# Kernel optimization log

Measured on AMD Instinct MI355X. Metric: run time of the kernel, lower is better.

The kernel has to match this reference:

```python
import jax, jax.numpy as jnp
import numpy as np
import math

B, S, K, D, H, LH, W, L = 8, 2048, 128, 512, 8, 4, 128, 4
DH = D // H           # 64, head dim
NW = S // W           # 16 windows
NUM_STEPS = 1000
RESCALE = 4000.0


def setup_inputs() -> dict:
    key = jax.random.key(0)
    ks = iter(jax.random.split(key, 48))
    def rn(shape, s=0.02):
        return jax.random.normal(next(ks), shape, dtype=jnp.float32) * s
    return {
        "x": jax.random.normal(next(ks), (B, S, K), dtype=jnp.float32),
        "t": jax.random.randint(next(ks), (B,), 0, NUM_STEPS, dtype=jnp.int32),
        "token_w": rn((K, D)), "token_b": jnp.zeros((D,), jnp.float32),
        "ax1": rn((NW, D), 1.0), "ax2": rn((W, D), 1.0),
        "time_w1": rn((D, 4 * D)), "time_b1": jnp.zeros((4 * D,), jnp.float32),
        "time_w2": rn((4 * D, D)), "time_b2": jnp.zeros((D,), jnp.float32),
        "ln1_g": jnp.ones((L, D), jnp.float32), "ln1_b": jnp.zeros((L, D), jnp.float32),
        "wq": rn((L, D, D)), "wk": rn((L, D, D)), "wv": rn((L, D, D)),
        "wo": rn((L, D, D)), "wo_b": jnp.zeros((L, D), jnp.float32),
        "ln2_g": jnp.ones((L, D), jnp.float32), "ln2_b": jnp.zeros((L, D), jnp.float32),
        "ff_w1": rn((L, D, 4 * D)), "ff_b1": jnp.zeros((L, 4 * D), jnp.float32),
        "ff_w2": rn((L, 4 * D, D)), "ff_b2": jnp.zeros((L, D), jnp.float32),
        "norm_g": jnp.ones((D,), jnp.float32), "norm_b": jnp.zeros((D,), jnp.float32),
        "out_w": rn((D, K)), "out_b": jnp.zeros((K,), jnp.float32),
        "alpha": jax.random.normal(next(ks), (1,), dtype=jnp.float32),
    }


def _layernorm(x, g, b, eps=1e-5):
    mu = x.mean(-1, keepdims=True)
    var = ((x - mu) ** 2).mean(-1, keepdims=True)
    return (x - mu) * jax.lax.rsqrt(var + eps) * g + b


def _mish(x):
    return x * jnp.tanh(jax.nn.softplus(x))


def _sinusoidal(t):
    # SinusoidalPosEmb(dim=D, num_steps=NUM_STEPS, rescale_steps=4000)
    tt = t.astype(jnp.float32) / NUM_STEPS * RESCALE
    half = D // 2
    freqs = jnp.exp(jnp.arange(half, dtype=jnp.float32) * (-math.log(10000.0) / (half - 1)))
    e = tt[:, None] * freqs[None, :]
    return jnp.concatenate([jnp.sin(e), jnp.cos(e)], axis=-1)  # (B, D)


def _linear_attn(q, k, v):
    # non-causal kernelized linear attention; q,k,v: (B, h, S, dh)
    scale = DH ** -0.25
    q = jax.nn.softmax(q * scale, axis=-1)   # softmax over feature dim
    k = jax.nn.softmax(k * scale, axis=-2)   # softmax over sequence dim
    ctx = jnp.einsum('bhnd,bhne->bhde', k, v)
    return jnp.einsum('bhnd,bhde->bhne', q, ctx)


def _local_attn(q, k, v):
    # windowed softmax attention, window W, look_backward=1, look_forward=1
    b, h = q.shape[0], q.shape[1]
    qw = q.reshape(b, h, NW, W, DH) * (DH ** -0.5)
    def look_around(x):
        xw = x.reshape(b, h, NW, W, DH)
        xp = jnp.pad(xw, ((0, 0), (0, 0), (1, 1), (0, 0), (0, 0)))
        # keys of windows [i-1, i, i+1] -> (b, h, NW, 3W, dh)
        return jnp.concatenate([xp[:, :, :-2], xp[:, :, 1:-1], xp[:, :, 2:]], axis=3)
    kw, vw = look_around(k), look_around(v)
    win = jnp.arange(NW)[:, None] + (jnp.arange(3 * W) // W)[None, :] - 1  # (NW, 3W)
    valid = (win >= 0) & (win < NW)
    dots = jnp.einsum('bhnwd,bhnkd->bhnwk', qw, kw)
    mask_value = -jnp.finfo(dots.dtype).max
    dots = jnp.where(valid[None, None, :, None, :], dots, mask_value)
    attn = jax.nn.softmax(dots, axis=-1)
    out = jnp.einsum('bhnwk,bhnkd->bhnwd', attn, vw)
    return out.reshape(b, h, S, DH)


def reference(x, t, token_w, token_b, ax1, ax2, time_w1, time_b1, time_w2, time_b2,
              ln1_g, ln1_b, wq, wk, wv, wo, wo_b, ln2_g, ln2_b,
              ff_w1, ff_b1, ff_w2, ff_b2, norm_g, norm_b, out_w, out_b, alpha):
    te = _sinusoidal(t)
    te = _mish(te @ time_w1 + time_b1) @ time_w2 + time_b2          # (B, D)
    h = x @ token_w + token_b                                        # token embedding
    pos = (ax1[:, None, :] + ax2[None, :, :]).reshape(S, D)          # axial pos emb (summed)
    h = h + pos[None] + te[:, None, :]
    for l in range(L):
        n = _layernorm(h, ln1_g[l], ln1_b[l])
        def split_heads(y):
            return y.reshape(B, S, H, DH).transpose(0, 2, 1, 3)
        q = split_heads(n @ wq[l]); k = split_heads(n @ wk[l]); v = split_heads(n @ wv[l])
        lo = _local_attn(q[:, :LH], k[:, :LH], v[:, :LH])            # local heads first
        gl = _linear_attn(q[:, LH:], k[:, LH:], v[:, LH:])           # global linear-attn heads
        a = jnp.concatenate([lo, gl], axis=1).transpose(0, 2, 1, 3).reshape(B, S, D)
        h = h + a @ wo[l] + wo_b[l]
        n = _layernorm(h, ln2_g[l], ln2_b[l])
        h = h + jax.nn.gelu(n @ ff_w1[l] + ff_b1[l], approximate=False) @ ff_w2[l] + ff_b2[l]
    out = _layernorm(h, norm_g, norm_b) @ out_w + out_b              # (B, S, K)
    return alpha * out.transpose(0, 2, 1)                            # permute + Rezero -> (B, K, S)
```

## Files before the change

### kernel.cpp

```cpp
#include <hip/hip_runtime.h>

typedef __bf16 bf16;
typedef float f32x4 __attribute__((ext_vector_type(4)));
typedef __bf16 b8v __attribute__((ext_vector_type(8)));
typedef __bf16 b4v __attribute__((ext_vector_type(4)));

#define S_LEN 2048
#define DMODEL 512
#define KDIM 128
#define NWIN 16
#define WIN 128
#define QKVS 1536

__device__ inline f32x4 mfma16(b8v a, b8v b, f32x4 c) {
  return __builtin_amdgcn_mfma_f32_16x16x32_bf16(a, b, c, 0, 0, 0);
}

__device__ inline void gload16(const bf16* g, bf16* l) {
  __builtin_amdgcn_global_load_lds(
      (const __attribute__((address_space(1))) void*)g,
      (__attribute__((address_space(3))) void*)l, 16, 0, 0);
}


__global__ __launch_bounds__(256) void conv_kernel(const float* __restrict__ in, bf16* __restrict__ out, int n) {
  int i4 = (blockIdx.x * 256 + threadIdx.x) * 4;
  if (i4 < n) {
    float4 v = *(const float4*)(in + i4);
    b4v o; o[0] = (bf16)v.x; o[1] = (bf16)v.y; o[2] = (bf16)v.z; o[3] = (bf16)v.w;
    *(b4v*)(out + i4) = o;
  }
}

__global__ __launch_bounds__(256) void convT_kernel(const float* __restrict__ W, bf16* __restrict__ WT,
                                                    int Kd, int N, size_t in_ls, size_t out_ls) {
  __shared__ float tile[32][33];
  int k0 = blockIdx.x * 32, n0 = blockIdx.y * 32;
  const float* Wl = W + (size_t)blockIdx.z * in_ls;
  bf16* WTl = WT + (size_t)blockIdx.z * out_ls;
  int tx = threadIdx.x & 31, ty = threadIdx.x >> 5;
  #pragma unroll
  for (int i = 0; i < 4; i++)
    tile[ty + i*8][tx] = Wl[(size_t)(k0 + ty + i*8) * N + n0 + tx];
  __syncthreads();
  #pragma unroll
  for (int i = 0; i < 4; i++)
    WTl[(size_t)(n0 + ty + i*8) * Kd + k0 + tx] = (bf16)tile[tx][ty + i*8];
}


__global__ __launch_bounds__(256) void time1_kernel(const int* __restrict__ t,
    const float* __restrict__ w1, const float* __restrict__ b1, float* __restrict__ te1) {
  __shared__ float te[512];
  __shared__ float red[4][64];
  int b = blockIdx.x >> 5;
  int c0 = (blockIdx.x & 31) * 64;
  int tid = threadIdx.x;
  float tt = (float)t[b] * 4.0f;
  {
    float fr = expf((float)tid * (-9.210340371976184f / 255.0f));
    float e = tt * fr;
    te[tid] = sinf(e);
    te[tid + 256] = cosf(e);
  }
  __syncthreads();
  int lane = tid & 63, wv = tid >> 6;
  float acc = 0.f;
  const float* wcol = w1 + (size_t)(wv * 128) * 2048 + c0 + lane;
  for (int dd = 0; dd < 128; dd++) acc = fmaf(te[wv * 128 + dd], wcol[(size_t)dd * 2048], acc);
  red[wv][lane] = acc;
  __syncthreads();
  if (tid < 64) {
    float a = red[0][tid] + red[1][tid] + red[2][tid] + red[3][tid] + b1[c0 + tid];
    float sp = (a > 20.f) ? a : log1pf(expf(a));
    te1[b * 2048 + c0 + tid] = a * tanhf(sp);
  }
}

__global__ __launch_bounds__(256) void time2_kernel(const float* __restrict__ te1,
    const float* __restrict__ w2, const float* __restrict__ b2, float* __restrict__ te2) {
  __shared__ float hb[2048];
  __shared__ float red[4][64];
  int b = blockIdx.x >> 3;
  int c0 = (blockIdx.x & 7) * 64;
  int tid = threadIdx.x;
  for (int i = tid; i < 2048; i += 256) hb[i] = te1[b * 2048 + i];
  __syncthreads();
  int lane = tid & 63, wv = tid >> 6;
  float acc = 0.f;
  const float* wcol = w2 + (size_t)(wv * 512) * 512 + c0 + lane;
  for (int dd = 0; dd < 512; dd++) acc = fmaf(hb[wv * 512 + dd], wcol[(size_t)dd * 512], acc);
  red[wv][lane] = acc;
  __syncthreads();
  if (tid < 64)
    te2[b * 512 + c0 + tid] = red[0][tid] + red[1][tid] + red[2][tid] + red[3][tid] + b2[c0 + tid];
}


__global__ __launch_bounds__(256) void ln_kernel(const float* __restrict__ hsrc,
    const float* __restrict__ gg, const float* __restrict__ bb, bf16* __restrict__ out) {
  int row = blockIdx.x * 4 + (threadIdx.x >> 6);
  int lane = threadIdx.x & 63;
  const float* hr = hsrc + (size_t)row * 512 + lane * 8;
  float4 v0 = *(const float4*)hr;
  float4 v1 = *(const float4*)(hr + 4);
  float xv[8] = {v0.x, v0.y, v0.z, v0.w, v1.x, v1.y, v1.z, v1.w};
  float s = 0.f;
  #pragma unroll
  for (int j = 0; j < 8; j++) s += xv[j];
  #pragma unroll
  for (int off = 1; off < 64; off <<= 1) s += __shfl_xor(s, off);
  float mu = s * (1.f / 512.f);
  float vs = 0.f;
  #pragma unroll
  for (int j = 0; j < 8; j++) { float dd = xv[j] - mu; vs += dd * dd; }
  #pragma unroll
  for (int off = 1; off < 64; off <<= 1) vs += __shfl_xor(vs, off);
  float rstd = 1.f / sqrtf(vs * (1.f / 512.f) + 1e-5f);
  int dbase = lane * 8;
  bf16* orow = out + (size_t)row * 512 + dbase;
  #pragma unroll
  for (int j = 0; j < 8; j++)
    orow[j] = (bf16)((xv[j] - mu) * rstd * gg[dbase + j] + bb[dbase + j]);
}

template<int EPI>
__global__ __launch_bounds__(256) void gemm_kernel(
    const bf16* __restrict__ A, const bf16* __restrict__ BT,
    const float* __restrict__ bias, float* __restrict__ Cf, bf16* __restrict__ Cb,
    int N, int Kd, int nbx,
    const float* __restrict__ q1, const float* __restrict__ q2, const float* __restrict__ q3,
    const float* __restrict__ alphap) {
  __shared__ bf16 As[2][4096];
  __shared__ bf16 Bs[2][4096];
  int tid = threadIdx.x;
  int lane = tid & 63, wid = tid >> 6;
  int g = lane >> 4, lr = lane & 15;
  int wm = wid >> 1, wn = wid & 1;
  int p = blockIdx.x;
  int cpx = (int)gridDim.x >> 3;
  int vid = (p & 7) * cpx + (p >> 3);
  int m0 = (vid / nbx) * 128;
  int n0 = (vid % nbx) * 128;
  f32x4 acc[4][4] = {};
  int srow = wid * 16 + (lane >> 2);
  int scol = (lane & 3) * 8;
  const bf16* pa = A + (size_t)(m0 + srow) * Kd + scol;
  const bf16* pb = BT + (size_t)(n0 + srow) * Kd + scol;
  const size_t rstep = (size_t)64 * Kd;
  int nt = Kd >> 5;
  auto stage = [&](int buf, int k0) {
    bf16* lA = &As[buf][wid * 512];
    bf16* lB = &Bs[buf][wid * 512];
    gload16(pa + k0, lA);
    gload16(pa + rstep + k0, lA + 2048);
    gload16(pb + k0, lB);
    gload16(pb + rstep + k0, lB + 2048);
  };
  stage(0, 0);
  __syncthreads();
  int cur = 0;
  for (int t = 0; t < nt; ++t) {
    if (t + 1 < nt) stage(cur ^ 1, (t + 1) * 32);
    b8v af[4], bfv[4];
    #pragma unroll
    for (int i = 0; i < 4; i++) af[i]  = *(const b8v*)&As[cur][(wm * 64 + i * 16 + lr) * 32 + g * 8];
    #pragma unroll
    for (int i = 0; i < 4; i++) bfv[i] = *(const b8v*)&Bs[cur][(wn * 64 + i * 16 + lr) * 32 + g * 8];
    #pragma unroll
    for (int mf = 0; mf < 4; mf++)
      #pragma unroll
      for (int nf = 0; nf < 4; nf++)
        acc[mf][nf] = mfma16(af[mf], bfv[nf], acc[mf][nf]);
    __syncthreads();
    cur ^= 1;
  }
  if constexpr (EPI == 4) {
    __shared__ float Ts[32][130];
    float alp = alphap[0];
    int b_ = m0 >> 11, sb = m0 & 2047;
    #pragma unroll
    for (int cg = 0; cg < 4; cg++) {
      __syncthreads();
      if (wn == (cg >> 1)) {
        #pragma unroll
        for (int nfi = 0; nfi < 2; nfi++) {
          int nf = (cg & 1) * 2 + nfi;
          int cl = nfi * 16 + lr;
          float bv = bias[cg * 32 + cl];
          #pragma unroll
          for (int mf = 0; mf < 4; mf++)
            #pragma unroll
            for (int r = 0; r < 4; r++)
              Ts[cl][wm * 64 + mf * 16 + g * 4 + r] = alp * (acc[mf][nf][r] + bv);
        }
      }
      __syncthreads();
      int cl = tid >> 3, soff = (tid & 7) * 16;
      int col = cg * 32 + cl;
      float* dst = Cf + (size_t)b_ * (KDIM * S_LEN) + (size_t)col * S_LEN + sb + soff;
      #pragma unroll
      for (int q4 = 0; q4 < 4; q4++) {
        float4 v = {Ts[cl][soff + q4*4], Ts[cl][soff + q4*4 + 1], Ts[cl][soff + q4*4 + 2], Ts[cl][soff + q4*4 + 3]};
        *(float4*)(dst + q4 * 4) = v;
      }
    }
    return;
  }
  #pragma unroll
  for (int mf = 0; mf < 4; mf++) {
    #pragma unroll
    for (int nf = 0; nf < 4; nf++) {
      int col = n0 + wn * 64 + nf * 16 + lr;
      float bv = (EPI != 0) ? bias[col] : 0.0f;
      #pragma unroll
      for (int r = 0; r < 4; r++) {
        int row = m0 + wm * 64 + mf * 16 + g * 4 + r;
        float v = acc[mf][nf][r] + bv;
        if (EPI == 0) {
          Cb[(size_t)row * N + col] = (bf16)v;
        } else if (EPI == 2) {
          Cf[(size_t)row * N + col] += v;
        } else if (EPI == 3) {
          float ge = 0.5f * v * (1.0f + erff(v * 0.70710678118654752f));
          Cb[(size_t)row * N + col] = (bf16)ge;
        } else if (EPI == 5) {
          int b_ = row >> 11, s_ = row & 2047;
          float pv = q1[(s_ >> 7) * 512 + col] + q2[(s_ & 127) * 512 + col] + q3[b_ * 512 + col];
          Cf[(size_t)row * N + col] = v + pv;
        }
      }
    }
  }
}

__global__ __launch_bounds__(256) void locattn_kernel(
    const bf16* __restrict__ qkv, bf16* __restrict__ ab) {
  __shared__ bf16 Ks[128][72];
  __shared__ bf16 Vt[64][136];
  __shared__ bf16 Ps[4][32][136];
  int w = blockIdx.x;
  int b = blockIdx.y >> 2, hh = blockIdx.y & 3;
  int tid = threadIdx.x, wid = tid >> 6, lane = tid & 63;
  int g = lane >> 4, lr = lane & 15;
  const size_t rowb = (size_t)b * S_LEN * QKVS;
  int qrow0 = w * WIN + wid * 32;
  b8v qf[2][2];
  #pragma unroll
  for (int mf = 0; mf < 2; mf++)
    #pragma unroll
    for (int kf = 0; kf < 2; kf++)
      qf[mf][kf] = *(const b8v*)(qkv + rowb + (size_t)(qrow0 + mf * 16 + lr) * QKVS + hh * 64 + kf * 32 + g * 8);
  float mrun[2][4], lrun[2][4];
  f32x4 oacc[2][4] = {};
  #pragma unroll
  for (int mf = 0; mf < 2; mf++)
    #pragma unroll
    for (int r = 0; r < 4; r++) { mrun[mf][r] = -3e38f; lrun[mf][r] = 0.f; }
  for (int c = 0; c < 3; c++) {
    int wc = w - 1 + c;
    if (wc < 0 || wc >= NWIN) continue;
    __syncthreads();
    {
      int row = tid >> 1, f0 = (tid & 1) * 32;
      const bf16* kp = qkv + rowb + (size_t)(wc * WIN + row) * QKVS + 512 + hh * 64 + f0;
      #pragma unroll
      for (int i = 0; i < 4; i++)
        *(b8v*)&Ks[row][f0 + i * 8] = *(const b8v*)(kp + i * 8);
      const bf16* vp = qkv + rowb + (size_t)(wc * WIN + row) * QKVS + 1024 + hh * 64 + f0;
      #pragma unroll
      for (int i = 0; i < 4; i++) {
        b8v vv = *(const b8v*)(vp + i * 8);
        #pragma unroll
        for (int j = 0; j < 8; j++) Vt[f0 + i * 8 + j][row] = vv[j];
      }
    }
    __syncthreads();
    f32x4 sc[2][8] = {};
    #pragma unroll
    for (int nf = 0; nf < 8; nf++) {
      #pragma unroll
      for (int kf = 0; kf < 2; kf++) {
        b8v kfr = *(const b8v*)&Ks[nf * 16 + lr][kf * 32 + g * 8];
        sc[0][nf] = mfma16(qf[0][kf], kfr, sc[0][nf]);
        sc[1][nf] = mfma16(qf[1][kf], kfr, sc[1][nf]);
      }
    }
    #pragma unroll
    for (int mf = 0; mf < 2; mf++) {
      #pragma unroll
      for (int r = 0; r < 4; r++) {
        float cm = -3e38f;
        #pragma unroll
        for (int nf = 0; nf < 8; nf++) { sc[mf][nf][r] *= 0.125f; cm = fmaxf(cm, sc[mf][nf][r]); }
        cm = fmaxf(cm, __shfl_xor(cm, 1));
        cm = fmaxf(cm, __shfl_xor(cm, 2));
        cm = fmaxf(cm, __shfl_xor(cm, 4));
        cm = fmaxf(cm, __shfl_xor(cm, 8));
        float mnew = fmaxf(mrun[mf][r], cm);
        float corr = __expf(mrun[mf][r] - mnew);
        float rs = 0.f;
        #pragma unroll
        for (int nf = 0; nf < 8; nf++) { float p = __expf(sc[mf][nf][r] - mnew); sc[mf][nf][r] = p; rs += p; }
        rs += __shfl_xor(rs, 1); rs += __shfl_xor(rs, 2);
        rs += __shfl_xor(rs, 4); rs += __shfl_xor(rs, 8);
        lrun[mf][r] = lrun[mf][r] * corr + rs;
        mrun[mf][r] = mnew;
        #pragma unroll
        for (int vf = 0; vf < 4; vf++) oacc[mf][vf][r] *= corr;
      }
    }
    #pragma unroll
    for (int mf = 0; mf < 2; mf++)
      #pragma unroll
      for (int nf = 0; nf < 8; nf++)
        #pragma unroll
        for (int r = 0; r < 4; r++)
          Ps[wid][mf * 16 + g * 4 + r][nf * 16 + lr] = (bf16)sc[mf][nf][r];
    #pragma unroll
    for (int kf2 = 0; kf2 < 4; kf2++) {
      b8v pa0 = *(const b8v*)&Ps[wid][lr][kf2 * 32 + g * 8];
      b8v pa1 = *(const b8v*)&Ps[wid][16 + lr][kf2 * 32 + g * 8];
      #pragma unroll
      for (int vf = 0; vf < 4; vf++) {
        b8v vv = *(const b8v*)&Vt[vf * 16 + lr][kf2 * 32 + g * 8];
        oacc[0][vf] = mfma16(pa0, vv, oacc[0][vf]);
        oacc[1][vf] = mfma16(pa1, vv, oacc[1][vf]);
      }
    }
  }
  #pragma unroll
  for (int mf = 0; mf < 2; mf++) {
    #pragma unroll
    for (int r = 0; r < 4; r++) {
      float inv = 1.0f / lrun[mf][r];
      int row = qrow0 + mf * 16 + g * 4 + r;
      #pragma unroll
      for (int vf = 0; vf < 4; vf++)
        ab[(size_t)b * S_LEN * DMODEL + (size_t)row * DMODEL + hh * 64 + vf * 16 + lr] = (bf16)(oacc[mf][vf][r] * inv);
    }
  }
}


__global__ __launch_bounds__(256) void la2_kernel(const bf16* __restrict__ qkv,
    float* __restrict__ part, float* __restrict__ psum) {
  int ch = blockIdx.x, bh = blockIdx.y;
  int b = bh >> 2, hh = bh & 3;
  __shared__ float ke[128][65];
  __shared__ float vsh[128][65];
  __shared__ float red[4][64];
  int tid = threadIdx.x;
  const float scale = 0.35355339059327373f;
  const size_t base = ((size_t)b * S_LEN + (size_t)ch * 128) * QKVS;
  const bf16* kp = qkv + base + 768 + hh * 64;
  const bf16* vp = qkv + base + 1280 + hh * 64;
  for (int i = tid; i < 1024; i += 256) {
    int s = i >> 3, d0 = (i & 7) * 8;
    b8v kv = *(const b8v*)(kp + (size_t)s * QKVS + d0);
    b8v vv = *(const b8v*)(vp + (size_t)s * QKVS + d0);
    #pragma unroll
    for (int j = 0; j < 8; j++) {
      ke[s][d0 + j] = __expf((float)kv[j] * scale);
      vsh[s][d0 + j] = (float)vv[j];
    }
  }
  __syncthreads();
  int d = tid & 63, sg = tid >> 6;
  float ps = 0.f;
  for (int s = sg * 32; s < sg * 32 + 32; s++) ps += ke[s][d];
  red[sg][d] = ps;
  int e = tid & 63, dg = tid >> 6;
  float accv[16] = {};
  for (int s = 0; s < 128; s++) {
    float vv2 = vsh[s][e];
    #pragma unroll
    for (int i = 0; i < 16; i++) accv[i] = fmaf(ke[s][dg * 16 + i], vv2, accv[i]);
  }
  __syncthreads();
  float* pp = part + ((size_t)ch * 32 + bh) * 4096 + (size_t)dg * 16 * 64 + e;
  #pragma unroll
  for (int i = 0; i < 16; i++) pp[i * 64] = accv[i];
  if (tid < 64)
    psum[((size_t)ch * 32 + bh) * 64 + tid] = red[0][tid] + red[1][tid] + red[2][tid] + red[3][tid];
}

__global__ __launch_bounds__(256) void la2b_kernel(const float* __restrict__ part,
    const float* __restrict__ psum, float* __restrict__ ctx) {
  int idx = blockIdx.x * 256 + threadIdx.x;
  int bh = idx >> 12;
  int d = (idx >> 6) & 63;
  float s = 0.f, cs = 0.f;
  for (int c = 0; c < 16; c++) {
    s += part[(size_t)c * 131072 + idx];
    cs += psum[(size_t)(c * 32 + bh) * 64 + d];
  }
  ctx[idx] = s / cs;
}

__global__ __launch_bounds__(256) void la3_kernel(const bf16* __restrict__ qkv,
    const float* __restrict__ ctx, bf16* __restrict__ ab) {
  int ch = blockIdx.x, bh = blockIdx.y;
  int b = bh >> 2, hh = bh & 3;
  __shared__ float cs[64][65];
  int tid = threadIdx.x;
  for (int i = tid; i < 4096; i += 256) cs[i >> 6][i & 63] = ctx[(size_t)bh * 4096 + i];
  __syncthreads();
  int s = ch * 128 + (tid >> 1);
  int e0 = (tid & 1) * 32;
  const float scale = 0.35355339059327373f;
  const bf16* qr = qkv + ((size_t)b * S_LEN + s) * QKVS + 256 + hh * 64;
  float qv[64];
  float mx = -3e38f;
  #pragma unroll
  for (int i = 0; i < 8; i++) {
    b8v qq = *(const b8v*)(qr + i * 8);
    #pragma unroll
    for (int j = 0; j < 8; j++) { qv[i * 8 + j] = (float)qq[j] * scale; mx = fmaxf(mx, qv[i * 8 + j]); }
  }
  float sum = 0.f;
  #pragma unroll
  for (int dd = 0; dd < 64; dd++) { qv[dd] = __expf(qv[dd] - mx); sum += qv[dd]; }
  float inv = 1.f / sum;
  float o[32] = {};
  #pragma unroll
  for (int dd = 0; dd < 64; dd++) {
    float qq = qv[dd] * inv;
    #pragma unroll
    for (int j = 0; j < 32; j++) o[j] = fmaf(qq, cs[dd][e0 + j], o[j]);
  }
  bf16* op = ab + ((size_t)b * S_LEN + s) * DMODEL + 256 + hh * 64 + e0;
  #pragma unroll
  for (int j = 0; j < 32; j++) op[j] = (bf16)o[j];
}


extern "C" void kernel_launch(void* const* d_in, const int* in_sizes, int n_in,
                              void* d_out, int out_size, void* d_ws, size_t ws_size,
                              hipStream_t stream) {
  (void)in_sizes; (void)n_in; (void)out_size; (void)ws_size;
  const float* x_f     = (const float*)d_in[0];
  const int*   t_i     = (const int*)  d_in[1];
  const float* token_w = (const float*)d_in[2];
  const float* token_b = (const float*)d_in[3];
  const float* ax1     = (const float*)d_in[4];
  const float* ax2     = (const float*)d_in[5];
  const float* time_w1 = (const float*)d_in[6];
  const float* time_b1 = (const float*)d_in[7];
  const float* time_w2 = (const float*)d_in[8];
  const float* time_b2 = (const float*)d_in[9];
  const float* ln1_g   = (const float*)d_in[10];
  const float* ln1_b   = (const float*)d_in[11];
  const float* wq      = (const float*)d_in[12];
  const float* wk      = (const float*)d_in[13];
  const float* wv      = (const float*)d_in[14];
  const float* wo      = (const float*)d_in[15];
  const float* wo_b    = (const float*)d_in[16];
  const float* ln2_g   = (const float*)d_in[17];
  const float* ln2_b   = (const float*)d_in[18];
  const float* ff_w1   = (const float*)d_in[19];
  const float* ff_b1   = (const float*)d_in[20];
  const float* ff_w2   = (const float*)d_in[21];
  const float* ff_b2   = (const float*)d_in[22];
  const float* norm_g  = (const float*)d_in[23];
  const float* norm_b  = (const float*)d_in[24];
  const float* out_w   = (const float*)d_in[25];
  const float* out_b   = (const float*)d_in[26];
  const float* alpha   = (const float*)d_in[27];

  char* ws = (char*)d_ws;
  float* h      = (float*)(ws + 0);
  float* te1    = (float*)(ws + 33554432);
  float* te2    = (float*)(ws + 33619968);
  float* psum   = (float*)(ws + 33636352);
  float* ctx    = (float*)(ws + 33767424);
  float* part   = (float*)(ws + 34291712);
  bf16* nbuf    = (bf16*)(ws + 42680320);
  bf16* qkvb    = (bf16*)(ws + 59457536);
  bf16* abuf    = (bf16*)(ws + 109789184);
  bf16* gbuf    = qkvb;
  bf16* xw      = (bf16*)(ws + 126566400);
  bf16* token_wT= (bf16*)(ws + 130760704);
  bf16* wqkvT   = (bf16*)(ws + 130891776);
  bf16* woT     = (bf16*)(ws + 137183232);
  bf16* ff1T    = (bf16*)(ws + 139280384);
  bf16* ff2T    = (bf16*)(ws + 147668992);
  bf16* outwT   = (bf16*)(ws + 156057600);

  conv_kernel<<<2048, 256, 0, stream>>>(x_f, xw, 2097152);
  convT_kernel<<<dim3(4, 16, 1),  256, 0, stream>>>(token_w, token_wT, 128, 512, 65536, 65536);
  convT_kernel<<<dim3(16, 16, 4), 256, 0, stream>>>(wq, wqkvT,           512, 512, 262144, 786432);
  convT_kernel<<<dim3(16, 16, 4), 256, 0, stream>>>(wk, wqkvT + 262144,  512, 512, 262144, 786432);
  convT_kernel<<<dim3(16, 16, 4), 256, 0, stream>>>(wv, wqkvT + 524288,  512, 512, 262144, 786432);
  convT_kernel<<<dim3(16, 16, 4), 256, 0, stream>>>(wo, woT, 512, 512, 262144, 262144);
  convT_kernel<<<dim3(16, 64, 4), 256, 0, stream>>>(ff_w1, ff1T, 512, 2048, 1048576, 1048576);
  convT_kernel<<<dim3(64, 16, 4), 256, 0, stream>>>(ff_w2, ff2T, 2048, 512, 1048576, 1048576);
  convT_kernel<<<dim3(16, 4, 1),  256, 0, stream>>>(out_w, outwT, 512, 128, 65536, 65536);

  time1_kernel<<<256, 256, 0, stream>>>(t_i, time_w1, time_b1, te1);
  time2_kernel<<<64, 256, 0, stream>>>(te1, time_w2, time_b2, te2);

  gemm_kernel<5><<<512, 256, 0, stream>>>(xw, token_wT, token_b, h, nullptr, 512, 128, 4, ax1, ax2, te2, nullptr);

  for (int l = 0; l < 4; l++) {
    ln_kernel<<<4096, 256, 0, stream>>>(h, ln1_g + l * 512, ln1_b + l * 512, nbuf);
    gemm_kernel<0><<<1536, 256, 0, stream>>>(nbuf, wqkvT + (size_t)l * 786432, nullptr, nullptr, qkvb, 1536, 512, 12, nullptr, nullptr, nullptr, nullptr);
    locattn_kernel<<<dim3(16, 32), 256, 0, stream>>>(qkvb, abuf);
    la2_kernel<<<dim3(16, 32), 256, 0, stream>>>(qkvb, part, psum);
    la2b_kernel<<<512, 256, 0, stream>>>(part, psum, ctx);
    la3_kernel<<<dim3(16, 32), 256, 0, stream>>>(qkvb, ctx, abuf);
    gemm_kernel<2><<<512, 256, 0, stream>>>(abuf, woT + (size_t)l * 262144, wo_b + l * 512, h, nullptr, 512, 512, 4, nullptr, nullptr, nullptr, nullptr);
    ln_kernel<<<4096, 256, 0, stream>>>(h, ln2_g + l * 512, ln2_b + l * 512, nbuf);
    gemm_kernel<3><<<2048, 256, 0, stream>>>(nbuf, ff1T + (size_t)l * 1048576, ff_b1 + l * 2048, nullptr, gbuf, 2048, 512, 16, nullptr, nullptr, nullptr, nullptr);
    gemm_kernel<2><<<512, 256, 0, stream>>>(gbuf, ff2T + (size_t)l * 1048576, ff_b2 + l * 512, h, nullptr, 512, 2048, 4, nullptr, nullptr, nullptr, nullptr);
  }

  ln_kernel<<<4096, 256, 0, stream>>>(h, norm_g, norm_b, nbuf);
  gemm_kernel<4><<<128, 256, 0, stream>>>(nbuf, outwT, out_b, (float*)d_out, nullptr, 128, 512, 1, nullptr, nullptr, nullptr, alpha);
}
```

Before: 1.212 ms.

## Add larger-tile 512-thread GEMM with triple-buffered async LDS pipeline

Adds a new templated GEMM that uses 8 waves per block, bigger output tiles (128x256 or 256x256) and a three-stage global-to-LDS ring buffer. It relies on raw vmcnt waits and a single barrier per K step, with XOR-swizzled LDS addressing and raised wave priority around the MFMA block. The per-layer QKV, output projection and FFN GEMMs are moved onto it, while the old GEMM is kept only for the embedding and output epilogues. The aim is to cut barrier and load latency stalls and raise data reuse per tile. In exchange, per-thread register use is higher and the grids are smaller, which can lower occupancy or leave CUs idle at the tail.

New measurement: 1.109 ms. 8.5% less time.

```diff
diff --git a/kernel.cpp b/kernel.cpp
--- a/kernel.cpp
+++ b/kernel.cpp
@@ -21,6 +21,10 @@
       (const __attribute__((address_space(1))) void*)g,
       (__attribute__((address_space(3))) void*)l, 16, 0, 0);
 }
+
+template<int N>
+__device__ inline void waitvm() { asm volatile("s_waitcnt vmcnt(%0)" :: "n"(N) : "memory"); }
+__device__ inline void barrier_raw() { asm volatile("s_barrier" ::: "memory"); }
 
 
 __global__ __launch_bounds__(256) void conv_kernel(const float* __restrict__ in, bf16* __restrict__ out, int n) {
@@ -122,6 +126,100 @@
   #pragma unroll
   for (int j = 0; j < 8; j++)
     orow[j] = (bf16)((xv[j] - mu) * rstd * gg[dbase + j] + bb[dbase + j]);
+}
+
+template<int EPI, int BM, int BN>
+__global__ __launch_bounds__(512, 2) void gemm2_kernel(
+    const bf16* __restrict__ A, const bf16* __restrict__ BT,
+    const float* __restrict__ bias, float* __restrict__ Cf, bf16* __restrict__ Cb,
+    int N, int Kd, int nbx) {
+  constexpr int LA = BM / 128;
+  constexpr int LB = BN / 128;
+  constexpr int LPI = LA + LB;
+  constexpr int EA = BM * 32;
+  constexpr int EB = BN * 32;
+  constexpr int ER = EA + EB;
+  constexpr int MF = BM / 32;
+  constexpr int NF = BN / 64;
+  __shared__ bf16 lds[ER * 3];
+  int tid = threadIdx.x;
+  int lane = tid & 63, wid = tid >> 6;
+  int g = lane >> 4, lr = lane & 15;
+  int wm = wid >> 2, wn = wid & 3;
+  int p = blockIdx.x;
+  int cpx = (int)gridDim.x >> 3;
+  int vid = (p & 7) * cpx + (p >> 3);
+  int m0 = (vid / nbx) * BM;
+  int n0 = (vid % nbx) * BN;
+  f32x4 acc[MF][NF] = {};
+  int rl = tid >> 2;
+  int csw = ((tid & 3) ^ ((rl >> 1) & 3)) * 8;
+  const bf16* pa = A + (size_t)(m0 + rl) * Kd + csw;
+  const bf16* pb = BT + (size_t)(n0 + rl) * Kd + csw;
+  int NT = Kd >> 5;
+  auto stage = [&](int t, int buf) {
+    int k0 = t << 5;
+    bf16* base = lds + buf * ER + (wid << 9);
+    #pragma unroll
+    for (int rr = 0; rr < LA; rr++)
+      gload16(pa + (size_t)(rr * 128) * Kd + k0, base + rr * 4096);
+    #pragma unroll
+    for (int rr = 0; rr < LB; rr++)
+      gload16(pb + (size_t)(rr * 128) * Kd + k0, base + EA + rr * 4096);
+  };
+  stage(0, 0);
+  stage(1, 1);
+  waitvm<LPI>();
+  barrier_raw();
+  for (int t = 0; t < NT; ++t) {
+    if (t + 2 < NT) stage(t + 2, (t + 2) % 3);
+    const bf16* ba = lds + (t % 3) * ER;
+    const bf16* bb = ba + EA;
+    b8v af[MF], bfr[NF];
+    #pragma unroll
+    for (int i = 0; i < MF; i++) {
+      int ra = wm * (BM / 2) + i * 16 + lr;
+      af[i] = *(const b8v*)(ba + ra * 32 + ((g * 8) ^ (((ra >> 1) & 3) << 3)));
+    }
+    #pragma unroll
+    for (int j = 0; j < NF; j++) {
+      int rb = wn * (BN / 4) + j * 16 + lr;
+      bfr[j] = *(const b8v*)(bb + rb * 32 + ((g * 8) ^ (((rb >> 1) & 3) << 3)));
+    }
+    __builtin_amdgcn_s_setprio(1);
+    #pragma unroll
+    for (int i = 0; i < MF; i++)
+      #pragma unroll
+      for (int j = 0; j < NF; j++)
+        acc[i][j] = mfma16(af[i], bfr[j], acc[i][j]);
+    __builtin_amdgcn_s_setprio(0);
+    if (t + 1 < NT) {
+      if (t + 2 < NT) waitvm<LPI>();
+      else            waitvm<0>();
+      barrier_raw();
+    }
+  }
+  #pragma unroll
+  for (int i = 0; i < MF; i++) {
+    #pragma unroll
+    for (int j = 0; j < NF; j++) {
+      int col = n0 + wn * (BN / 4) + j * 16 + lr;
+      float bv = (EPI != 0) ? bias[col] : 0.0f;
+      #pragma unroll
+      for (int r = 0; r < 4; r++) {
+        int row = m0 + wm * (BM / 2) + i * 16 + g * 4 + r;
+        float v = acc[i][j][r] + bv;
+        if (EPI == 0) {
+          Cb[(size_t)row * N + col] = (bf16)v;
+        } else if (EPI == 2) {
+          Cf[(size_t)row * N + col] += v;
+        } else if (EPI == 3) {
+          float ge = 0.5f * v * (1.0f + erff(v * 0.70710678118654752f));
+          Cb[(size_t)row * N + col] = (bf16)ge;
+        }
+      }
+    }
+  }
 }
 
 template<int EPI>
@@ -212,19 +310,12 @@
     #pragma unroll
     for (int nf = 0; nf < 4; nf++) {
       int col = n0 + wn * 64 + nf * 16 + lr;
-      float bv = (EPI != 0) ? bias[col] : 0.0f;
+      float bv = bias[col];
       #pragma unroll
       for (int r = 0; r < 4; r++) {
         int row = m0 + wm * 64 + mf * 16 + g * 4 + r;
         float v = acc[mf][nf][r] + bv;
-        if (EPI == 0) {
-          Cb[(size_t)row * N + col] = (bf16)v;
-        } else if (EPI == 2) {
-          Cf[(size_t)row * N + col] += v;
-        } else if (EPI == 3) {
-          float ge = 0.5f * v * (1.0f + erff(v * 0.70710678118654752f));
-          Cb[(size_t)row * N + col] = (bf16)ge;
-        } else if (EPI == 5) {
+        if (EPI == 5) {
           int b_ = row >> 11, s_ = row & 2047;
           float pv = q1[(s_ >> 7) * 512 + col] + q2[(s_ & 127) * 512 + col] + q3[b_ * 512 + col];
           Cf[(size_t)row * N + col] = v + pv;
@@ -504,15 +595,15 @@
 
   for (int l = 0; l < 4; l++) {
     ln_kernel<<<4096, 256, 0, stream>>>(h, ln1_g + l * 512, ln1_b + l * 512, nbuf);
-    gemm_kernel<0><<<1536, 256, 0, stream>>>(nbuf, wqkvT + (size_t)l * 786432, nullptr, nullptr, qkvb, 1536, 512, 12, nullptr, nullptr, nullptr, nullptr);
+    gemm2_kernel<0, 128, 256><<<768, 512, 0, stream>>>(nbuf, wqkvT + (size_t)l * 786432, nullptr, nullptr, qkvb, 1536, 512, 6);
     locattn_kernel<<<dim3(16, 32), 256, 0, stream>>>(qkvb, abuf);
     la2_kernel<<<dim3(16, 32), 256, 0, stream>>>(qkvb, part, psum);
     la2b_kernel<<<512, 256, 0, stream>>>(part, psum, ctx);
     la3_kernel<<<dim3(16, 32), 256, 0, stream>>>(qkvb, ctx, abuf);
-    gemm_kernel<2><<<512, 256, 0, stream>>>(abuf, woT + (size_t)l * 262144, wo_b + l * 512, h, nullptr, 512, 512, 4, nullptr, nullptr, nullptr, nullptr);
+    gemm2_kernel<2, 128, 256><<<256, 512, 0, stream>>>(abuf, woT + (size_t)l * 262144, wo_b + l * 512, h, nullptr, 512, 512, 2);
     ln_kernel<<<4096, 256, 0, stream>>>(h, ln2_g + l * 512, ln2_b + l * 512, nbuf);
-    gemm_kernel<3><<<2048, 256, 0, stream>>>(nbuf, ff1T + (size_t)l * 1048576, ff_b1 + l * 2048, nullptr, gbuf, 2048, 512, 16, nullptr, nullptr, nullptr, nullptr);
-    gemm_kernel<2><<<512, 256, 0, stream>>>(gbuf, ff2T + (size_t)l * 1048576, ff_b2 + l * 512, h, nullptr, 512, 2048, 4, nullptr, nullptr, nullptr, nullptr);
+    gemm2_kernel<3, 256, 256><<<512, 512, 0, stream>>>(nbuf, ff1T + (size_t)l * 1048576, ff_b1 + l * 2048, nullptr, gbuf, 2048, 512, 8);
+    gemm2_kernel<2, 128, 256><<<256, 512, 0, stream>>>(gbuf, ff2T + (size_t)l * 1048576, ff_b2 + l * 512, h, nullptr, 512, 2048, 2);
   }
 
   ln_kernel<<<4096, 256, 0, stream>>>(h, norm_g, norm_b, nbuf);
```

## Add larger-tile 512-thread GEMM with phased prefetch for per-layer matmuls

Applied to the files above, without the earlier changes.

Adds a new GEMM kernel that uses 512 threads, 128 or 256 by 256 output tiles, and double-buffered async global-to-LDS loads. The next tile's loads are interleaved with compute phases, and raw barriers plus s_setprio raise MFMA priority. All per-layer GEMMs (QKV, output projection, FF1, FF2) switch to it to get more data reuse per block and better load/compute overlap. The FF1 epilogue also swaps the erf GELU for a tanh-style sigmoid approximation, which trades a small accuracy loss for cheaper math. Larger tiles mean fewer blocks, so some GEMMs may underfill the 256 CUs.

Result: faster. 1.122 ms (-7.5%).

```diff
diff --git a/kernel.cpp b/kernel.cpp
--- a/kernel.cpp
+++ b/kernel.cpp
@@ -21,6 +21,10 @@
       (const __attribute__((address_space(1))) void*)g,
       (__attribute__((address_space(3))) void*)l, 16, 0, 0);
 }
+
+template<int N>
+__device__ inline void waitvm() { asm volatile("s_waitcnt vmcnt(%0)" :: "n"(N) : "memory"); }
+__device__ inline void barrier_raw() { asm volatile("s_barrier" ::: "memory"); }
 
 
 __global__ __launch_bounds__(256) void conv_kernel(const float* __restrict__ in, bf16* __restrict__ out, int n) {
@@ -122,6 +126,112 @@
   #pragma unroll
   for (int j = 0; j < 8; j++)
     orow[j] = (bf16)((xv[j] - mu) * rstd * gg[dbase + j] + bb[dbase + j]);
+}
+
+template<int EPI, int BM>
+__global__ __launch_bounds__(512, 1) void gemm5_kernel(
+    const bf16* __restrict__ A, const bf16* __restrict__ BT,
+    const float* __restrict__ bias, float* __restrict__ Cf, bf16* __restrict__ Cb,
+    int N, int Kd, int nbx) {
+  constexpr int MF  = BM / 32;
+  constexpr int NPH = MF / 2;
+  constexpr int UA  = BM / 64;
+  constexpr int AE  = BM * 64;
+  constexpr int BE  = 256 * 64;
+  constexpr int TE  = AE + BE;
+  __shared__ bf16 lds[TE * 2];
+  int tid = threadIdx.x, lane = tid & 63, wid = tid >> 6;
+  int g = lane >> 4, lr = lane & 15;
+  int wm = wid >> 2, wn = wid & 3;
+  int p = blockIdx.x, cpx = (int)gridDim.x >> 3;
+  int vid = (p & 7) * cpx + (p >> 3);
+  int m0 = (vid / nbx) * BM, n0 = (vid % nbx) * 256;
+  f32x4 acc[MF][4] = {};
+  int riu = wid * 8 + (lane >> 3);
+  int scol = ((lane & 7) ^ (riu & 7)) << 3;
+  const bf16* pa = A + (size_t)(m0 + riu) * Kd + scol;
+  const bf16* pb = BT + (size_t)(n0 + riu) * Kd + scol;
+  int NT = Kd >> 6;
+  auto stA = [&](int t, int u) {
+    gload16(pa + (size_t)(u * 64) * Kd + t * 64,
+            lds + (t & 1) * TE + u * 4096 + (wid << 9));
+  };
+  auto stB = [&](int t, int u) {
+    gload16(pb + (size_t)(u * 64) * Kd + t * 64,
+            lds + (t & 1) * TE + AE + u * 4096 + (wid << 9));
+  };
+  #pragma unroll
+  for (int u = 0; u < UA; u++) stA(0, u);
+  #pragma unroll
+  for (int u = 0; u < 4; u++) stB(0, u);
+  for (int t = 0; t < NT; ++t) {
+    const bf16* ba = lds + (t & 1) * TE;
+    const bf16* bb = ba + AE;
+    waitvm<0>();
+    barrier_raw();
+    b8v bfr[4][2], af[2][2];
+    bool more = (t + 1 < NT);
+    #pragma unroll
+    for (int ph = 0; ph < NPH; ph++) {
+      if (more) {
+        if constexpr (BM == 256) {
+          stA(t + 1, ph); stB(t + 1, ph);
+        } else {
+          if (ph == 0) { stA(t + 1, 0); stA(t + 1, 1); stB(t + 1, 0); }
+          else         { stB(t + 1, 1); stB(t + 1, 2); stB(t + 1, 3); }
+        }
+      }
+      if (ph == 0) {
+        #pragma unroll
+        for (int j = 0; j < 4; j++) {
+          int br = wn * 64 + j * 16 + lr;
+          #pragma unroll
+          for (int kk = 0; kk < 2; kk++)
+            bfr[j][kk] = *(const b8v*)(bb + br * 64 + ((((kk << 2) + g) ^ (br & 7)) << 3));
+        }
+      }
+      #pragma unroll
+      for (int i2 = 0; i2 < 2; i2++) {
+        int ar = wm * (BM / 2) + (2 * ph + i2) * 16 + lr;
+        #pragma unroll
+        for (int kk = 0; kk < 2; kk++)
+          af[i2][kk] = *(const b8v*)(ba + ar * 64 + ((((kk << 2) + g) ^ (ar & 7)) << 3));
+      }
+      barrier_raw();
+      __builtin_amdgcn_s_setprio(1);
+      #pragma unroll
+      for (int i2 = 0; i2 < 2; i2++)
+        #pragma unroll
+        for (int j = 0; j < 4; j++)
+          #pragma unroll
+          for (int kk = 0; kk < 2; kk++)
+            acc[2 * ph + i2][j] = mfma16(af[i2][kk], bfr[j][kk], acc[2 * ph + i2][j]);
+      __builtin_amdgcn_s_setprio(0);
+      barrier_raw();
+    }
+  }
+  #pragma unroll
+  for (int i = 0; i < MF; i++) {
+    #pragma unroll
+    for (int j = 0; j < 4; j++) {
+      int col = n0 + wn * 64 + j * 16 + lr;
+      float bv = (EPI != 0) ? bias[col] : 0.0f;
+      #pragma unroll
+      for (int r = 0; r < 4; r++) {
+        int row = m0 + wm * (BM / 2) + i * 16 + g * 4 + r;
+        float v = acc[i][j][r] + bv;
+        if (EPI == 0) {
+          Cb[(size_t)row * N + col] = (bf16)v;
+        } else if (EPI == 2) {
+          Cf[(size_t)row * N + col] += v;
+        } else if (EPI == 3) {
+          float u = 1.5957691216057308f * (v + 0.044715f * v * v * v);
+          float ge = v / (1.0f + __expf(-u));
+          Cb[(size_t)row * N + col] = (bf16)ge;
+        }
+      }
+    }
+  }
 }
 
 template<int EPI>
@@ -212,19 +322,12 @@
     #pragma unroll
     for (int nf = 0; nf < 4; nf++) {
       int col = n0 + wn * 64 + nf * 16 + lr;
-      float bv = (EPI != 0) ? bias[col] : 0.0f;
+      float bv = bias[col];
       #pragma unroll
       for (int r = 0; r < 4; r++) {
         int row = m0 + wm * 64 + mf * 16 + g * 4 + r;
         float v = acc[mf][nf][r] + bv;
-        if (EPI == 0) {
-          Cb[(size_t)row * N + col] = (bf16)v;
-        } else if (EPI == 2) {
-          Cf[(size_t)row * N + col] += v;
-        } else if (EPI == 3) {
-          float ge = 0.5f * v * (1.0f + erff(v * 0.70710678118654752f));
-          Cb[(size_t)row * N + col] = (bf16)ge;
-        } else if (EPI == 5) {
+        if (EPI == 5) {
           int b_ = row >> 11, s_ = row & 2047;
           float pv = q1[(s_ >> 7) * 512 + col] + q2[(s_ & 127) * 512 + col] + q3[b_ * 512 + col];
           Cf[(size_t)row * N + col] = v + pv;
@@ -504,15 +607,15 @@
 
   for (int l = 0; l < 4; l++) {
     ln_kernel<<<4096, 256, 0, stream>>>(h, ln1_g + l * 512, ln1_b + l * 512, nbuf);
-    gemm_kernel<0><<<1536, 256, 0, stream>>>(nbuf, wqkvT + (size_t)l * 786432, nullptr, nullptr, qkvb, 1536, 512, 12, nullptr, nullptr, nullptr, nullptr);
+    gemm5_kernel<0, 128><<<768, 512, 0, stream>>>(nbuf, wqkvT + (size_t)l * 786432, nullptr, nullptr, qkvb, 1536, 512, 6);
     locattn_kernel<<<dim3(16, 32), 256, 0, stream>>>(qkvb, abuf);
     la2_kernel<<<dim3(16, 32), 256, 0, stream>>>(qkvb, part, psum);
     la2b_kernel<<<512, 256, 0, stream>>>(part, psum, ctx);
     la3_kernel<<<dim3(16, 32), 256, 0, stream>>>(qkvb, ctx, abuf);
-    gemm_kernel<2><<<512, 256, 0, stream>>>(abuf, woT + (size_t)l * 262144, wo_b + l * 512, h, nullptr, 512, 512, 4, nullptr, nullptr, nullptr, nullptr);
+    gemm5_kernel<2, 128><<<256, 512, 0, stream>>>(abuf, woT + (size_t)l * 262144, wo_b + l * 512, h, nullptr, 512, 512, 2);
     ln_kernel<<<4096, 256, 0, stream>>>(h, ln2_g + l * 512, ln2_b + l * 512, nbuf);
-    gemm_kernel<3><<<2048, 256, 0, stream>>>(nbuf, ff1T + (size_t)l * 1048576, ff_b1 + l * 2048, nullptr, gbuf, 2048, 512, 16, nullptr, nullptr, nullptr, nullptr);
-    gemm_kernel<2><<<512, 256, 0, stream>>>(gbuf, ff2T + (size_t)l * 1048576, ff_b2 + l * 512, h, nullptr, 512, 2048, 4, nullptr, nullptr, nullptr, nullptr);
+    gemm5_kernel<3, 256><<<512, 512, 0, stream>>>(nbuf, ff1T + (size_t)l * 1048576, ff_b1 + l * 2048, nullptr, gbuf, 2048, 512, 8);
+    gemm5_kernel<2, 128><<<256, 512, 0, stream>>>(gbuf, ff2T + (size_t)l * 1048576, ff_b2 + l * 512, h, nullptr, 512, 2048, 2);
   }
 
   ln_kernel<<<4096, 256, 0, stream>>>(h, norm_g, norm_b, nbuf);
```
